# Kernel optimization log

Hardware: AMD Instinct MI355X
Metric: run time of the kernel (lower is better)

The kernel has to match this reference:

```python
import jax, jax.numpy as jnp
import numpy as np

FEAT = 512
ACT_NUMS = (8, 6, 4)            # actions per categorical type
SUM_ACT = sum(ACT_NUMS)          # 18
STARTS = np.cumsum([0] + list(ACT_NUMS[:-1]))  # [0, 8, 14]
FC_HIDDEN, FC_OUT = 140, 256


def setup_inputs() -> dict:
    key = jax.random.key(0)
    ks = jax.random.split(key, 10)
    F, A = 2048, 32
    s = 0.02
    return {
        "current_feature": jax.random.normal(ks[0], (F, A, FEAT), jnp.float32),
        "next_feature": jax.random.normal(ks[1], (F, A, FEAT), jnp.float32),
        "actions": jax.random.randint(ks[2], (F, 3, A), 0, 4),
        "W1": jax.random.normal(ks[3], (FEAT + SUM_ACT, FC_HIDDEN), jnp.float32) * s,
        "b1": jnp.zeros((FC_HIDDEN,), jnp.float32),
        "W2": jax.random.normal(ks[4], (FC_HIDDEN, FC_OUT), jnp.float32) * s,
        "b2": jnp.zeros((FC_OUT,), jnp.float32),
        "Wi0": jax.random.normal(ks[5], (2 * FEAT, ACT_NUMS[0]), jnp.float32) * s,
        "bi0": jnp.zeros((ACT_NUMS[0],), jnp.float32),
        "Wi1": jax.random.normal(ks[6], (2 * FEAT, ACT_NUMS[1]), jnp.float32) * s,
        "bi1": jnp.zeros((ACT_NUMS[1],), jnp.float32),
        "Wi2": jax.random.normal(ks[7], (2 * FEAT, ACT_NUMS[2]), jnp.float32) * s,
        "bi2": jnp.zeros((ACT_NUMS[2],), jnp.float32),
    }


def reference(current_feature, next_feature, actions,
              W1, b1, W2, b2, Wi0, bi0, Wi1, bi1, Wi2, bi2):
    dt = current_feature.dtype
    starts = jnp.asarray(STARTS, dtype=actions.dtype)  # [3]
    # Vectorized replacement of the triple nested scatter loop:
    # global index per (frame, type, agent), one-hot over SUM_ACT, summed over types
    # (per-type index ranges are disjoint, so sum == set).
    idx = actions + starts[None, :, None]                       # [F, T, A]
    action_one_hot = jax.nn.one_hot(idx, SUM_ACT, dtype=dt).sum(axis=1)  # [F, A, S]

    # Forward dynamics: fwd_net = Linear -> Linear (no nonlinearity, per source)
    fwd_in = jnp.concatenate([current_feature, action_one_hot], axis=2)  # [F, A, FEAT+S]
    next_feature_pred = (fwd_in @ W1 + b1) @ W2 + b2                     # [F, A, 256]

    # Inverse dynamics: per-action-type Linear + Softmax(dim=1)
    # (nn.Softmax(dim=1) on a 3D tensor normalizes over the agent axis -- kept faithful)
    inv_in = jnp.concatenate([current_feature, next_feature], axis=2)    # [F, A, 2*FEAT]
    a0 = jax.nn.softmax(inv_in @ Wi0 + bi0, axis=1)
    a1 = jax.nn.softmax(inv_in @ Wi1 + bi1, axis=1)
    a2 = jax.nn.softmax(inv_in @ Wi2 + bi2, axis=1)
    return (next_feature_pred, a0, a1, a2)
```

## Files before the change

kernel.cpp:

```cpp
#include <hip/hip_runtime.h>


using bf16x8  = __attribute__((ext_vector_type(8))) __bf16;
using floatx4 = __attribute__((ext_vector_type(4))) float;

__device__ __forceinline__ unsigned short f2bf(float f) {
    unsigned int u = __float_as_uint(f);
    return (unsigned short)((u + 0x7fffu + ((u >> 16) & 1u)) >> 16);
}
__device__ __forceinline__ bf16x8 cvt8r(float4 x, float4 y) {
    union { bf16x8 v; unsigned short s[8]; } u;
    u.s[0] = f2bf(x.x); u.s[1] = f2bf(x.y); u.s[2] = f2bf(x.z); u.s[3] = f2bf(x.w);
    u.s[4] = f2bf(y.x); u.s[5] = f2bf(y.y); u.s[6] = f2bf(y.z); u.s[7] = f2bf(y.w);
    return u.v;
}

#define OFF_W1P 0
#define OFF_W2P (OFF_W1P + 16*9*512)
#define OFF_WCP (OFF_W2P + 5*16*512)

#define OFF_A0 ((size_t)16777216)
#define OFF_A1 ((size_t)17301504)
#define OFF_A2 ((size_t)17694720)

__global__ __launch_bounds__(256) void prep_kernel(
    const float* __restrict__ W1,
    const float* __restrict__ W2,
    const float* __restrict__ Wi0,
    const float* __restrict__ Wi1,
    const float* __restrict__ Wi2,
    unsigned short* __restrict__ ws)
{
    const int T1 = 16*9*512;
    const int T2 = T1 + 5*16*512;
    const int total = T2 + 32*2*512;
    for (int idx = blockIdx.x * 256 + threadIdx.x; idx < total; idx += gridDim.x * 256) {
        unsigned short v = 0;
        if (idx < T1) {
            int e = idx & 7, l = (idx >> 3) & 63;
            int n = (idx >> 9) % 9, kc = idx / (9*512);
            int k = kc*32 + ((l >> 4) << 3) + e, j = n*16 + (l & 15);
            if (j < 140) v = f2bf(W1[k*140 + j]);
            ws[OFF_W1P + idx] = v;
        } else if (idx < T2) {
            int i2 = idx - T1;
            int e = i2 & 7, l = (i2 >> 3) & 63;
            int n = (i2 >> 9) & 15, kc = i2 >> 13;
            int k = kc*32 + ((l >> 4) << 3) + e, j = n*16 + (l & 15);
            if (k < 140) v = f2bf(W2[k*256 + j]);
            ws[OFF_W2P + i2] = v;
        } else {
            int i3 = idx - T2;
            int e = i3 & 7, l = (i3 >> 3) & 63;
            int n = (i3 >> 9) & 1, kc = i3 >> 10;
            int k = kc*32 + ((l >> 4) << 3) + e, j = n*16 + (l & 15);
            if (j < 8)       v = f2bf(Wi0[k*8 + j]);
            else if (j < 14) v = f2bf(Wi1[k*6 + (j - 8)]);
            else if (j < 18) v = f2bf(Wi2[k*4 + (j - 14)]);
            ws[OFF_WCP + i3] = v;
        }
    }
}

__global__ __launch_bounds__(256) void fused_kernel(
    const float* __restrict__ cf,
    const float* __restrict__ nf,
    const int* __restrict__ actions,
    const float* __restrict__ W1,
    const float* __restrict__ b1,
    const float* __restrict__ b2,
    const unsigned short* __restrict__ ws,
    float* __restrict__ outp)
{
    __shared__ alignas(16) __bf16 hs[64 * 168];
    __shared__ float Us[18 * 144];
    __shared__ float b1s[144];
    __shared__ float b2s[256];
    __shared__ float Ls[64 * 20];
    __shared__ float rmx[36], rsc[36];
    __shared__ int   sidx[192];

    const int t = threadIdx.x, w = t >> 6, l = t & 63;
    const int m0 = blockIdx.x * 64;
    const int q = l >> 4, col = l & 15;
    const unsigned short* W1P = ws + OFF_W1P;
    const unsigned short* W2P = ws + OFF_W2P;
    const unsigned short* WCP = ws + OFF_WCP;

    {
        float uv[11];
#pragma unroll
        for (int it = 0; it < 11; ++it) {
            int i = t + it * 256;
            uv[it] = 0.f;
            if (i < 18 * 144) {
                int s = i / 144, j = i - s * 144;
                if (j < 140) uv[it] = W1[(512 + s) * 140 + j];
            }
        }
        float bv1 = (t < 140) ? b1[t] : 0.f;
        float bv2 = b2[t];
        int sv = 0;
        if (t < 192) {
            int r = t / 3, tt = t - r * 3;
            int m = m0 + r;
            int start = (tt == 0) ? 0 : (tt == 1 ? 8 : 14);
            sv = actions[(m >> 5) * 96 + tt * 32 + (m & 31)] + start;
        }
#pragma unroll
        for (int it = 0; it < 11; ++it) {
            int i = t + it * 256;
            if (i < 18 * 144) Us[i] = uv[it];
        }
        if (t < 144) b1s[t] = bv1;
        b2s[t] = bv2;
        if (t < 192) sidx[t] = sv;
    }

    const float* cfr = cf + (size_t)(m0 + w * 16 + col) * 512 + q * 8;
    const float* nfr = nf + (size_t)(m0 + w * 16 + col) * 512 + q * 8;

    floatx4 acc1[9], acc3[2];
#pragma unroll
    for (int n = 0; n < 9; ++n) { acc1[n][0]=0.f; acc1[n][1]=0.f; acc1[n][2]=0.f; acc1[n][3]=0.f; }
#pragma unroll
    for (int n = 0; n < 2; ++n) { acc3[n][0]=0.f; acc3[n][1]=0.f; acc3[n][2]=0.f; acc3[n][3]=0.f; }

    const int base = blockIdx.x & 15;

    {
        float4 c0 = *(const float4*)(cfr + base * 32);
        float4 c1 = *(const float4*)(cfr + base * 32 + 4);
        for (int i = 0; i < 16; ++i) {
            const int kc  = (base + i) & 15;
            const int kn  = (base + i + 1) & 15;
            float4 n0 = *(const float4*)(cfr + kn * 32);
            float4 n1 = *(const float4*)(cfr + kn * 32 + 4);
            bf16x8 av = cvt8r(c0, c1);
            const unsigned short* bp = W1P + (size_t)(kc * 9) * 512 + l * 8;
#pragma unroll
            for (int n = 0; n < 9; ++n)
                acc1[n] = __builtin_amdgcn_mfma_f32_16x16x32_bf16(
                    av, *(const bf16x8*)(bp + n * 512), acc1[n], 0, 0, 0);
            const unsigned short* cp = WCP + (size_t)(kc * 2) * 512 + l * 8;
            acc3[0] = __builtin_amdgcn_mfma_f32_16x16x32_bf16(
                av, *(const bf16x8*)(cp), acc3[0], 0, 0, 0);
            acc3[1] = __builtin_amdgcn_mfma_f32_16x16x32_bf16(
                av, *(const bf16x8*)(cp + 512), acc3[1], 0, 0, 0);
            c0 = n0; c1 = n1;
        }
    }

    {
        float4 c0 = *(const float4*)(nfr + base * 32);
        float4 c1 = *(const float4*)(nfr + base * 32 + 4);
        for (int i = 0; i < 16; ++i) {
            const int kc  = (base + i) & 15;
            const int kn  = (base + i + 1) & 15;
            float4 n0 = *(const float4*)(nfr + kn * 32);
            float4 n1 = *(const float4*)(nfr + kn * 32 + 4);
            bf16x8 av = cvt8r(c0, c1);
            const unsigned short* cp = WCP + (size_t)((16 + kc) * 2) * 512 + l * 8;
            acc3[0] = __builtin_amdgcn_mfma_f32_16x16x32_bf16(
                av, *(const bf16x8*)(cp), acc3[0], 0, 0, 0);
            acc3[1] = __builtin_amdgcn_mfma_f32_16x16x32_bf16(
                av, *(const bf16x8*)(cp + 512), acc3[1], 0, 0, 0);
            c0 = n0; c1 = n1;
        }
    }

    __syncthreads();

    const int r0 = w * 16 + (q << 2);
#pragma unroll
    for (int i = 0; i < 4; ++i) {
        int rr = r0 + i;
        int s0 = sidx[rr * 3], s1 = sidx[rr * 3 + 1], s2 = sidx[rr * 3 + 2];
#pragma unroll
        for (int n = 0; n < 9; ++n) {
            int j = n * 16 + col;
            float v = acc1[n][i] + b1s[j] + Us[s0 * 144 + j] + Us[s1 * 144 + j] + Us[s2 * 144 + j];
            ((unsigned short*)hs)[rr * 168 + j] = f2bf(v);
        }
    }
    {
        int rr = t >> 2, g = t & 3;
        ushort4 z; z.x = z.y = z.z = z.w = 0;
        *(ushort4*)((unsigned short*)hs + rr * 168 + 144 + g * 4) = z;
    }
#pragma unroll
    for (int n = 0; n < 2; ++n) {
        int j = n * 16 + col;
        if (j < 18) {
#pragma unroll
            for (int i = 0; i < 4; ++i) Ls[(r0 + i) * 20 + j] = acc3[n][i];
        }
    }
    __syncthreads();

    floatx4 acc2[16];
#pragma unroll
    for (int n = 0; n < 16; ++n) { acc2[n][0]=0.f; acc2[n][1]=0.f; acc2[n][2]=0.f; acc2[n][3]=0.f; }

    for (int kc = 0; kc < 5; ++kc) {
        bf16x8 av = *(const bf16x8*)&hs[(w * 16 + col) * 168 + kc * 32 + q * 8];
        const unsigned short* bp = W2P + (size_t)(kc * 16) * 512 + l * 8;
#pragma unroll
        for (int n = 0; n < 16; ++n)
            acc2[n] = __builtin_amdgcn_mfma_f32_16x16x32_bf16(
                av, *(const bf16x8*)(bp + n * 512), acc2[n], 0, 0, 0);
    }
#pragma unroll
    for (int n = 0; n < 16; ++n) {
        int j = n * 16 + col;
        float bj = b2s[j];
#pragma unroll
        for (int i = 0; i < 4; ++i)
            outp[(size_t)(m0 + r0 + i) * 256 + j] = acc2[n][i] + bj;
    }

    if (t < 36) {
        int fr = t / 18, j = t - fr * 18;
        float mx = -1e30f;
        for (int a = 0; a < 32; ++a) mx = fmaxf(mx, Ls[(fr * 32 + a) * 20 + j]);
        float s = 0.f;
        for (int a = 0; a < 32; ++a) s += expf(Ls[(fr * 32 + a) * 20 + j] - mx);
        rmx[t] = mx; rsc[t] = 1.f / s;
    }
    __syncthreads();

#pragma unroll
    for (int it = 0; it < 5; ++it) {
        int idx = t + it * 256;
        if (idx < 1152) {
            int r = idx / 18, j = idx - r * 18;
            int fr = r >> 5;
            float v = expf(Ls[r * 20 + j] - rmx[fr * 18 + j]) * rsc[fr * 18 + j];
            int m = m0 + r;
            size_t o;
            if (j < 8)       o = OFF_A0 + (size_t)m * 8 + j;
            else if (j < 14) o = OFF_A1 + (size_t)m * 6 + (j - 8);
            else             o = OFF_A2 + (size_t)m * 4 + (j - 14);
            outp[o] = v;
        }
    }
}

extern "C" void kernel_launch(void* const* d_in, const int* in_sizes, int n_in,
                              void* d_out, int out_size, void* d_ws, size_t ws_size,
                              hipStream_t stream)
{
    const float* cf  = (const float*)d_in[0];
    const float* nf  = (const float*)d_in[1];
    const int*   act = (const int*)d_in[2];
    const float* W1  = (const float*)d_in[3];
    const float* b1  = (const float*)d_in[4];
    const float* W2  = (const float*)d_in[5];
    const float* b2  = (const float*)d_in[6];
    const float* Wi0 = (const float*)d_in[7];
    const float* Wi1 = (const float*)d_in[9];
    const float* Wi2 = (const float*)d_in[11];

    unsigned short* ws = (unsigned short*)d_ws;
    float* outp = (float*)d_out;

    hipLaunchKernelGGL(prep_kernel, dim3(144), dim3(256), 0, stream,
                       W1, W2, Wi0, Wi1, Wi2, ws);
    hipLaunchKernelGGL(fused_kernel, dim3(1024), dim3(256), 0, stream,
                       cf, nf, act, W1, b1, b2, ws, outp);
}
```

Measured before the change: 364.9 us.

## Merge current/next feature K-loops with two-deep register prefetch and sched barriers

Combines the two separate K loops over current_feature and next_feature into one loop that processes both per K-chunk. Activation loads are prefetched two chunks ahead with alternating register sets, and weight loads are issued up front behind sched_barriers so that global loads overlap the MFMA chains. The aim is to hide global-memory latency on the streamed activations. The cost is higher register pressure, which could lower occupancy or cause spills.

```diff
diff --git a/kernel.cpp b/kernel.cpp
--- a/kernel.cpp
+++ b/kernel.cpp
@@ -62,6 +62,46 @@
     }
 }
 
+#define MFMA16(av, bv, acc) __builtin_amdgcn_mfma_f32_16x16x32_bf16(av, bv, acc, 0, 0, 0)
+
+#define SECTION(X0, X1, Y0, Y1, KC, KP, PRE) do {                              \
+    bf16x8 avc = cvt8r(X0, X1);                                                \
+    bf16x8 avn = cvt8r(Y0, Y1);                                                \
+    const unsigned short* bp = W1P + (size_t)((KC) * 9) * 512 + lo8;           \
+    bf16x8 w0 = *(const bf16x8*)(bp);                                          \
+    bf16x8 w1 = *(const bf16x8*)(bp + 512);                                    \
+    bf16x8 w2 = *(const bf16x8*)(bp + 1024);                                   \
+    bf16x8 w3 = *(const bf16x8*)(bp + 1536);                                   \
+    bf16x8 w4 = *(const bf16x8*)(bp + 2048);                                   \
+    bf16x8 w5 = *(const bf16x8*)(bp + 2560);                                   \
+    bf16x8 w6 = *(const bf16x8*)(bp + 3072);                                   \
+    bf16x8 w7 = *(const bf16x8*)(bp + 3584);                                   \
+    bf16x8 w8 = *(const bf16x8*)(bp + 4096);                                   \
+    __builtin_amdgcn_sched_barrier(0);                                         \
+    if (PRE) {                                                                 \
+        X0 = *(const float4*)(cfr + (KP) * 32);                                \
+        X1 = *(const float4*)(cfr + (KP) * 32 + 4);                            \
+        Y0 = *(const float4*)(nfr + (KP) * 32);                                \
+        Y1 = *(const float4*)(nfr + (KP) * 32 + 4);                            \
+        __builtin_amdgcn_sched_barrier(0);                                     \
+    }                                                                          \
+    acc1[0] = MFMA16(avc, w0, acc1[0]);                                        \
+    acc1[1] = MFMA16(avc, w1, acc1[1]);                                        \
+    acc1[2] = MFMA16(avc, w2, acc1[2]);                                        \
+    acc1[3] = MFMA16(avc, w3, acc1[3]);                                        \
+    acc1[4] = MFMA16(avc, w4, acc1[4]);                                        \
+    acc1[5] = MFMA16(avc, w5, acc1[5]);                                        \
+    acc1[6] = MFMA16(avc, w6, acc1[6]);                                        \
+    acc1[7] = MFMA16(avc, w7, acc1[7]);                                        \
+    acc1[8] = MFMA16(avc, w8, acc1[8]);                                        \
+    const unsigned short* cpc = WCP + (size_t)((KC) * 2) * 512 + lo8;          \
+    const unsigned short* cpn = WCP + (size_t)((16 + (KC)) * 2) * 512 + lo8;   \
+    acc3[0] = MFMA16(avc, *(const bf16x8*)(cpc), acc3[0]);                     \
+    acc3[1] = MFMA16(avc, *(const bf16x8*)(cpc + 512), acc3[1]);               \
+    acc3[0] = MFMA16(avn, *(const bf16x8*)(cpn), acc3[0]);                     \
+    acc3[1] = MFMA16(avn, *(const bf16x8*)(cpn + 512), acc3[1]);               \
+} while (0)
+
 __global__ __launch_bounds__(256) void fused_kernel(
     const float* __restrict__ cf,
     const float* __restrict__ nf,
@@ -83,6 +123,7 @@
     const int t = threadIdx.x, w = t >> 6, l = t & 63;
     const int m0 = blockIdx.x * 64;
     const int q = l >> 4, col = l & 15;
+    const int lo8 = l * 8;
     const unsigned short* W1P = ws + OFF_W1P;
     const unsigned short* W2P = ws + OFF_W2P;
     const unsigned short* WCP = ws + OFF_WCP;
@@ -129,44 +170,22 @@
     const int base = blockIdx.x & 15;
 
     {
-        float4 c0 = *(const float4*)(cfr + base * 32);
-        float4 c1 = *(const float4*)(cfr + base * 32 + 4);
-        for (int i = 0; i < 16; ++i) {
-            const int kc  = (base + i) & 15;
-            const int kn  = (base + i + 1) & 15;
-            float4 n0 = *(const float4*)(cfr + kn * 32);
-            float4 n1 = *(const float4*)(cfr + kn * 32 + 4);
-            bf16x8 av = cvt8r(c0, c1);
-            const unsigned short* bp = W1P + (size_t)(kc * 9) * 512 + l * 8;
-#pragma unroll
-            for (int n = 0; n < 9; ++n)
-                acc1[n] = __builtin_amdgcn_mfma_f32_16x16x32_bf16(
-                    av, *(const bf16x8*)(bp + n * 512), acc1[n], 0, 0, 0);
-            const unsigned short* cp = WCP + (size_t)(kc * 2) * 512 + l * 8;
-            acc3[0] = __builtin_amdgcn_mfma_f32_16x16x32_bf16(
-                av, *(const bf16x8*)(cp), acc3[0], 0, 0, 0);
-            acc3[1] = __builtin_amdgcn_mfma_f32_16x16x32_bf16(
-                av, *(const bf16x8*)(cp + 512), acc3[1], 0, 0, 0);
-            c0 = n0; c1 = n1;
-        }
-    }
-
-    {
-        float4 c0 = *(const float4*)(nfr + base * 32);
-        float4 c1 = *(const float4*)(nfr + base * 32 + 4);
-        for (int i = 0; i < 16; ++i) {
-            const int kc  = (base + i) & 15;
-            const int kn  = (base + i + 1) & 15;
-            float4 n0 = *(const float4*)(nfr + kn * 32);
-            float4 n1 = *(const float4*)(nfr + kn * 32 + 4);
-            bf16x8 av = cvt8r(c0, c1);
-            const unsigned short* cp = WCP + (size_t)((16 + kc) * 2) * 512 + l * 8;
-            acc3[0] = __builtin_amdgcn_mfma_f32_16x16x32_bf16(
-                av, *(const bf16x8*)(cp), acc3[0], 0, 0, 0);
-            acc3[1] = __builtin_amdgcn_mfma_f32_16x16x32_bf16(
-                av, *(const bf16x8*)(cp + 512), acc3[1], 0, 0, 0);
-            c0 = n0; c1 = n1;
-        }
+        const int kA = base, kB = (base + 1) & 15;
+        float4 xa0 = *(const float4*)(cfr + kA * 32);
+        float4 xa1 = *(const float4*)(cfr + kA * 32 + 4);
+        float4 ya0 = *(const float4*)(nfr + kA * 32);
+        float4 ya1 = *(const float4*)(nfr + kA * 32 + 4);
+        float4 xb0 = *(const float4*)(cfr + kB * 32);
+        float4 xb1 = *(const float4*)(cfr + kB * 32 + 4);
+        float4 yb0 = *(const float4*)(nfr + kB * 32);
+        float4 yb1 = *(const float4*)(nfr + kB * 32 + 4);
+
+        for (int i = 0; i < 14; i += 2) {
+            SECTION(xa0, xa1, ya0, ya1, ((base + i)     & 15), ((base + i + 2) & 15), 1);
+            SECTION(xb0, xb1, yb0, yb1, ((base + i + 1) & 15), ((base + i + 3) & 15), 1);
+        }
+        SECTION(xa0, xa1, ya0, ya1, ((base + 14) & 15), 0, 0);
+        SECTION(xb0, xb1, yb0, yb1, ((base + 15) & 15), 0, 0);
     }
 
     __syncthreads();
@@ -204,7 +223,7 @@
 
     for (int kc = 0; kc < 5; ++kc) {
         bf16x8 av = *(const bf16x8*)&hs[(w * 16 + col) * 168 + kc * 32 + q * 8];
-        const unsigned short* bp = W2P + (size_t)(kc * 16) * 512 + l * 8;
+        const unsigned short* bp = W2P + (size_t)(kc * 16) * 512 + lo8;
 #pragma unroll
         for (int n = 0; n < 16; ++n)
             acc2[n] = __builtin_amdgcn_mfma_f32_16x16x32_bf16(
```

Result: faster. 347.1 us (-4.9%).

## Stage weight fragments in LDS shared by all waves and fuse cf/nf loops

Applied to the files above, without the earlier changes.

Each of the four waves now loads a quarter of the per-k-chunk weight fragments (W1 plus the inverse-dynamics weights) from global memory into a shared LDS buffer, and all waves read them back. Before, every wave fetched all fragments itself. The current- and next-feature K loops are merged into one unrolled loop with double-buffered activation loads. The second GEMM is split into two halves of 8 accumulators to reduce register pressure. This cuts redundant global/L2 weight traffic, but adds two block barriers per k-chunk and extra LDS round trips.

```diff
diff --git a/kernel.cpp b/kernel.cpp
--- a/kernel.cpp
+++ b/kernel.cpp
@@ -62,6 +62,8 @@
     }
 }
 
+#define MFMA16(av, bv, acc) __builtin_amdgcn_mfma_f32_16x16x32_bf16(av, bv, acc, 0, 0, 0)
+
 __global__ __launch_bounds__(256) void fused_kernel(
     const float* __restrict__ cf,
     const float* __restrict__ nf,
@@ -72,7 +74,7 @@
     const unsigned short* __restrict__ ws,
     float* __restrict__ outp)
 {
-    __shared__ alignas(16) __bf16 hs[64 * 168];
+    __shared__ alignas(16) unsigned short fragbuf[64 * 168];
     __shared__ float Us[18 * 144];
     __shared__ float b1s[144];
     __shared__ float b2s[256];
@@ -83,6 +85,7 @@
     const int t = threadIdx.x, w = t >> 6, l = t & 63;
     const int m0 = blockIdx.x * 64;
     const int q = l >> 4, col = l & 15;
+    const int lo8 = l * 8;
     const unsigned short* W1P = ws + OFF_W1P;
     const unsigned short* W2P = ws + OFF_W2P;
     const unsigned short* WCP = ws + OFF_WCP;
@@ -128,95 +131,145 @@
 
     const int base = blockIdx.x & 15;
 
+    auto fsrc = [&](int kn, int sl) -> const unsigned short* {
+        if (sl < 9)  return W1P + (size_t)(kn * 9 + sl) * 512 + lo8;
+        if (sl < 11) return WCP + (size_t)(kn * 2 + (sl - 9)) * 512 + lo8;
+        return WCP + (size_t)((16 + kn) * 2 + (sl - 11)) * 512 + lo8;
+    };
+
     {
-        float4 c0 = *(const float4*)(cfr + base * 32);
-        float4 c1 = *(const float4*)(cfr + base * 32 + 4);
+        const int sl0 = w, sl1 = w + 4, sl2 = w + 8;
+        bf16x8 r0, r1, r2, r3;
+        r0 = *(const bf16x8*)fsrc(base, sl0);
+        r1 = *(const bf16x8*)fsrc(base, sl1);
+        r2 = *(const bf16x8*)fsrc(base, sl2);
+        r3 = r0;
+        if (w == 0) r3 = *(const bf16x8*)fsrc(base, 12);
+        float4 ax0, ax1, ay0, ay1, bx0, bx1, by0, by1;
+        ax0 = *(const float4*)(cfr + base * 32);
+        ax1 = *(const float4*)(cfr + base * 32 + 4);
+        ay0 = *(const float4*)(nfr + base * 32);
+        ay1 = *(const float4*)(nfr + base * 32 + 4);
+        bx0 = ax0; bx1 = ax1; by0 = ay0; by1 = ay1;
+
+#pragma unroll
         for (int i = 0; i < 16; ++i) {
-            const int kc  = (base + i) & 15;
-            const int kn  = (base + i + 1) & 15;
-            float4 n0 = *(const float4*)(cfr + kn * 32);
-            float4 n1 = *(const float4*)(cfr + kn * 32 + 4);
-            bf16x8 av = cvt8r(c0, c1);
-            const unsigned short* bp = W1P + (size_t)(kc * 9) * 512 + l * 8;
-#pragma unroll
-            for (int n = 0; n < 9; ++n)
-                acc1[n] = __builtin_amdgcn_mfma_f32_16x16x32_bf16(
-                    av, *(const bf16x8*)(bp + n * 512), acc1[n], 0, 0, 0);
-            const unsigned short* cp = WCP + (size_t)(kc * 2) * 512 + l * 8;
-            acc3[0] = __builtin_amdgcn_mfma_f32_16x16x32_bf16(
-                av, *(const bf16x8*)(cp), acc3[0], 0, 0, 0);
-            acc3[1] = __builtin_amdgcn_mfma_f32_16x16x32_bf16(
-                av, *(const bf16x8*)(cp + 512), acc3[1], 0, 0, 0);
-            c0 = n0; c1 = n1;
-        }
-    }
-
-    {
-        float4 c0 = *(const float4*)(nfr + base * 32);
-        float4 c1 = *(const float4*)(nfr + base * 32 + 4);
-        for (int i = 0; i < 16; ++i) {
-            const int kc  = (base + i) & 15;
-            const int kn  = (base + i + 1) & 15;
-            float4 n0 = *(const float4*)(nfr + kn * 32);
-            float4 n1 = *(const float4*)(nfr + kn * 32 + 4);
-            bf16x8 av = cvt8r(c0, c1);
-            const unsigned short* cp = WCP + (size_t)((16 + kc) * 2) * 512 + l * 8;
-            acc3[0] = __builtin_amdgcn_mfma_f32_16x16x32_bf16(
-                av, *(const bf16x8*)(cp), acc3[0], 0, 0, 0);
-            acc3[1] = __builtin_amdgcn_mfma_f32_16x16x32_bf16(
-                av, *(const bf16x8*)(cp + 512), acc3[1], 0, 0, 0);
-            c0 = n0; c1 = n1;
-        }
-    }
-
-    __syncthreads();
-
-    const int r0 = w * 16 + (q << 2);
+            {
+                unsigned short* fd = fragbuf + lo8;
+                *(bf16x8*)(fd + sl0 * 512) = r0;
+                *(bf16x8*)(fd + sl1 * 512) = r1;
+                *(bf16x8*)(fd + sl2 * 512) = r2;
+                if (w == 0) *(bf16x8*)(fd + 12 * 512) = r3;
+            }
+            if (i < 15) {
+                const int kn = (base + i + 1) & 15;
+                r0 = *(const bf16x8*)fsrc(kn, sl0);
+                r1 = *(const bf16x8*)fsrc(kn, sl1);
+                r2 = *(const bf16x8*)fsrc(kn, sl2);
+                if (w == 0) r3 = *(const bf16x8*)fsrc(kn, 12);
+                if ((i & 1) == 0) {
+                    bx0 = *(const float4*)(cfr + kn * 32);
+                    bx1 = *(const float4*)(cfr + kn * 32 + 4);
+                    by0 = *(const float4*)(nfr + kn * 32);
+                    by1 = *(const float4*)(nfr + kn * 32 + 4);
+                } else {
+                    ax0 = *(const float4*)(cfr + kn * 32);
+                    ax1 = *(const float4*)(cfr + kn * 32 + 4);
+                    ay0 = *(const float4*)(nfr + kn * 32);
+                    ay1 = *(const float4*)(nfr + kn * 32 + 4);
+                }
+            }
+            __syncthreads();
+
+            {
+                const unsigned short* fs = fragbuf + lo8;
+                float4 cx0 = ((i & 1) == 0) ? ax0 : bx0;
+                float4 cx1 = ((i & 1) == 0) ? ax1 : bx1;
+                float4 cy0 = ((i & 1) == 0) ? ay0 : by0;
+                float4 cy1 = ((i & 1) == 0) ? ay1 : by1;
+                bf16x8 avc = cvt8r(cx0, cx1);
+                bf16x8 avn = cvt8r(cy0, cy1);
+                bf16x8 f0 = *(const bf16x8*)(fs + 0 * 512);
+                bf16x8 f1 = *(const bf16x8*)(fs + 1 * 512);
+                bf16x8 f2 = *(const bf16x8*)(fs + 2 * 512);
+                bf16x8 f3 = *(const bf16x8*)(fs + 3 * 512);
+                bf16x8 f4 = *(const bf16x8*)(fs + 4 * 512);
+                bf16x8 f5 = *(const bf16x8*)(fs + 5 * 512);
+                bf16x8 f6 = *(const bf16x8*)(fs + 6 * 512);
+                bf16x8 f7 = *(const bf16x8*)(fs + 7 * 512);
+                bf16x8 f8 = *(const bf16x8*)(fs + 8 * 512);
+                bf16x8 c0 = *(const bf16x8*)(fs + 9 * 512);
+                bf16x8 c1 = *(const bf16x8*)(fs + 10 * 512);
+                bf16x8 c2 = *(const bf16x8*)(fs + 11 * 512);
+                bf16x8 c3 = *(const bf16x8*)(fs + 12 * 512);
+                acc1[0] = MFMA16(avc, f0, acc1[0]);
+                acc1[1] = MFMA16(avc, f1, acc1[1]);
+                acc1[2] = MFMA16(avc, f2, acc1[2]);
+                acc1[3] = MFMA16(avc, f3, acc1[3]);
+                acc1[4] = MFMA16(avc, f4, acc1[4]);
+                acc1[5] = MFMA16(avc, f5, acc1[5]);
+                acc1[6] = MFMA16(avc, f6, acc1[6]);
+                acc1[7] = MFMA16(avc, f7, acc1[7]);
+                acc1[8] = MFMA16(avc, f8, acc1[8]);
+                acc3[0] = MFMA16(avc, c0, acc3[0]);
+                acc3[1] = MFMA16(avc, c1, acc3[1]);
+                acc3[0] = MFMA16(avn, c2, acc3[0]);
+                acc3[1] = MFMA16(avn, c3, acc3[1]);
+            }
+            __syncthreads();
+        }
+    }
+
+    const int r0w = w * 16 + (q << 2);
 #pragma unroll
     for (int i = 0; i < 4; ++i) {
-        int rr = r0 + i;
+        int rr = r0w + i;
         int s0 = sidx[rr * 3], s1 = sidx[rr * 3 + 1], s2 = sidx[rr * 3 + 2];
 #pragma unroll
         for (int n = 0; n < 9; ++n) {
             int j = n * 16 + col;
             float v = acc1[n][i] + b1s[j] + Us[s0 * 144 + j] + Us[s1 * 144 + j] + Us[s2 * 144 + j];
-            ((unsigned short*)hs)[rr * 168 + j] = f2bf(v);
+            fragbuf[rr * 168 + j] = f2bf(v);
         }
     }
     {
         int rr = t >> 2, g = t & 3;
         ushort4 z; z.x = z.y = z.z = z.w = 0;
-        *(ushort4*)((unsigned short*)hs + rr * 168 + 144 + g * 4) = z;
+        *(ushort4*)(fragbuf + rr * 168 + 144 + g * 4) = z;
     }
 #pragma unroll
     for (int n = 0; n < 2; ++n) {
         int j = n * 16 + col;
         if (j < 18) {
 #pragma unroll
-            for (int i = 0; i < 4; ++i) Ls[(r0 + i) * 20 + j] = acc3[n][i];
+            for (int i = 0; i < 4; ++i) Ls[(r0w + i) * 20 + j] = acc3[n][i];
         }
     }
     __syncthreads();
 
-    floatx4 acc2[16];
-#pragma unroll
-    for (int n = 0; n < 16; ++n) { acc2[n][0]=0.f; acc2[n][1]=0.f; acc2[n][2]=0.f; acc2[n][3]=0.f; }
-
-    for (int kc = 0; kc < 5; ++kc) {
-        bf16x8 av = *(const bf16x8*)&hs[(w * 16 + col) * 168 + kc * 32 + q * 8];
-        const unsigned short* bp = W2P + (size_t)(kc * 16) * 512 + l * 8;
-#pragma unroll
-        for (int n = 0; n < 16; ++n)
-            acc2[n] = __builtin_amdgcn_mfma_f32_16x16x32_bf16(
-                av, *(const bf16x8*)(bp + n * 512), acc2[n], 0, 0, 0);
-    }
-#pragma unroll
-    for (int n = 0; n < 16; ++n) {
-        int j = n * 16 + col;
-        float bj = b2s[j];
-#pragma unroll
-        for (int i = 0; i < 4; ++i)
-            outp[(size_t)(m0 + r0 + i) * 256 + j] = acc2[n][i] + bj;
+    {
+        const unsigned short* hsp = fragbuf;
+#pragma unroll 1
+        for (int half = 0; half < 2; ++half) {
+            floatx4 acc2[8];
+#pragma unroll
+            for (int n = 0; n < 8; ++n) { acc2[n][0]=0.f; acc2[n][1]=0.f; acc2[n][2]=0.f; acc2[n][3]=0.f; }
+            for (int kc = 0; kc < 5; ++kc) {
+                bf16x8 av = *(const bf16x8*)(hsp + (w * 16 + col) * 168 + kc * 32 + q * 8);
+                const unsigned short* bp = W2P + (size_t)(kc * 16 + half * 8) * 512 + lo8;
+#pragma unroll
+                for (int n = 0; n < 8; ++n)
+                    acc2[n] = MFMA16(av, *(const bf16x8*)(bp + n * 512), acc2[n]);
+            }
+#pragma unroll
+            for (int n = 0; n < 8; ++n) {
+                int j = (half * 8 + n) * 16 + col;
+                float bj = b2s[j];
+#pragma unroll
+                for (int i = 0; i < 4; ++i)
+                    outp[(size_t)(m0 + r0w + i) * 256 + j] = acc2[n][i] + bj;
+            }
+        }
     }
 
     if (t < 36) {
```

Result: faster. 343.4 us (-5.9%).
